# Optimization experiments

Measured on AMD Instinct MI355X. Metric: run time of the kernel, lower is better.

Reference implementation:

```python
import jax, jax.numpy as jnp
import numpy as np

B, C_IN, N_IN, N_OUT = 4, 64, 8192, 8192
D1, F, H = 4, 15, 16384  # d+1, filter_size, max_hash_cnt
C_MID, C_OUT = 64, 64
LEAK = 0.01


def setup_inputs() -> dict:
    key = jax.random.key(0)
    ks = jax.random.split(key, 10)
    features = jax.random.normal(ks[0], (B, C_IN, N_IN), jnp.float32)
    in_barycentric = jax.random.uniform(ks[1], (B, D1, N_IN), dtype=jnp.float32)
    # global flat lattice offsets: local vertex id in [0,H) plus per-batch base b*(H+1)
    local_off = jax.random.randint(ks[2], (B, D1, N_IN), 0, H)
    base = (jnp.arange(B, dtype=jnp.int64) * (H + 1))[:, None, None]
    in_lattice_offset = local_off.astype(jnp.int64) + base
    # neighbor ids in [-1, H); -1 means missing -> maps to zero padding slot after +1
    blur_neighbors = (jax.random.randint(ks[3], (B, F, H), 0, H + 1) - 1).astype(jnp.int64)
    out_barycentric = jax.random.uniform(ks[4], (B, D1, N_OUT), dtype=jnp.float32)
    out_lattice_offset = jax.random.randint(ks[5], (B, D1, N_OUT), 0, H).astype(jnp.int64)
    # blur conv params: layer0 Conv2d(C_IN,C_MID,(F,1)) + LeakyReLU, layer1 Conv2d(C_MID,C_OUT,(1,1)) no relu
    W0 = jax.random.normal(ks[6], (C_MID, C_IN, F), jnp.float32) * 0.05
    b0 = jax.random.normal(ks[7], (C_MID,), jnp.float32) * 0.01
    W1 = jax.random.normal(ks[8], (C_OUT, C_MID), jnp.float32) * 0.1
    b1 = jax.random.normal(ks[9], (C_OUT,), jnp.float32) * 0.01
    bias = jnp.zeros((C_OUT,), jnp.float32)  # slice bias, initialized to zeros as in module
    return dict(features=features, in_barycentric=in_barycentric,
                in_lattice_offset=in_lattice_offset, blur_neighbors=blur_neighbors,
                out_barycentric=out_barycentric, out_lattice_offset=out_lattice_offset,
                W0=W0, b0=b0, W1=W1, b1=b1, bias=bias)


def reference(features, in_barycentric, in_lattice_offset, blur_neighbors,
              out_barycentric, out_lattice_offset, W0, b0, W1, b1, bias):
    b_sz, c_in, n_in = features.shape
    max_hash = blur_neighbors.shape[-1]
    # ---- splat: scatter-sum barycentric-weighted features onto lattice vertices ----
    vals = in_barycentric[:, None, :, :] * features[:, :, None, :]      # (B,C,d1,N)
    vals = vals.transpose(0, 2, 3, 1).reshape(-1, c_in)                  # (B*d1*N, C)
    idx = (in_lattice_offset + 1).reshape(-1)                            # (B*d1*N,)
    splat = jax.ops.segment_sum(vals, idx, num_segments=b_sz * (max_hash + 1))
    splat = splat.reshape(b_sz, max_hash + 1, c_in).transpose(0, 2, 1)   # (B,C,H+1)
    # normalization: splat of all-ones feature
    one_splat = jax.ops.segment_sum(in_barycentric.reshape(-1), idx,
                                    num_segments=b_sz * (max_hash + 1))
    one_splat = one_splat.reshape(b_sz, max_hash + 1)
    splat = splat / (one_splat + 1e-5)[:, None, :]
    # ---- blur: gather F neighbors per vertex, then conv over the filter axis ----
    spread = jax.vmap(lambda s, n: s[:, n])(splat, blur_neighbors + 1)   # (B,C,F,H)
    h0 = jnp.einsum('bcfh,ocf->boh', spread, W0) + b0[None, :, None]     # (B,C_mid,H)
    h0 = jnp.where(h0 > 0, h0, LEAK * h0)                                # LeakyReLU
    feat_blurred = jnp.einsum('boh,po->bph', h0, W1) + b1[None, :, None] # (B,C_out,H)
    # ---- slice: barycentric-weighted gather back to output points ----
    tmp = jax.vmap(lambda f, o: f[:, o])(feat_blurred, out_lattice_offset)  # (B,C_out,d1,N_out)
    sliced = (out_barycentric[:, None, :, :] * tmp).sum(axis=2)
    sliced = sliced + bias[None, :, None]
    return sliced
```

## Files before the change

### kernel.cpp

```cpp
#include <hip/hip_runtime.h>

#define NB 4
#define C_IN 64
#define N_IN 8192
#define N_OUT 8192
#define D1 4
#define FS 15
#define HSZ 16384
#define C_MID 64
#define C_OUT 64
#define LEAK 0.01f
#define CAP 24

#define NVERT (NB*(HSZ+1))

typedef __attribute__((ext_vector_type(8))) short short8;
typedef __attribute__((ext_vector_type(4))) float floatx4;

#define SPLATB_OFF 0
#define SPLATB_FL  (NVERT*32)
#define W0B_OFF    (SPLATB_OFF + SPLATB_FL)
#define W0B_FL     (C_MID*C_IN*FS/2)
#define W1B_OFF    (W0B_OFF + W0B_FL)
#define W1B_FL     (C_OUT*C_MID/2)
#define BREG_OFF   (W1B_OFF + W1B_FL)
#define FEATB_OFF  (BREG_OFF)
#define FEATB_FL   (NB*N_IN*32)
#define CNT_OFF    (FEATB_OFF + FEATB_FL)
#define CNT_FL     (NVERT)
#define ENTID_OFF  (CNT_OFF + CNT_FL)
#define ENT_FL     (NVERT*CAP)
#define ENTW_OFF   (ENTID_OFF + ENT_FL)
#define FB_OFF     (BREG_OFF)
#define FB_FL      (NB*HSZ*32)

__device__ inline ushort f2bf(float x) {
    uint u = __float_as_uint(x);
    return (ushort)((u + 0x7FFF + ((u >> 16) & 1)) >> 16);
}
__device__ inline float bf2f(ushort b) {
    return __uint_as_float(((uint)b) << 16);
}

__global__ __launch_bounds__(256) void transpose_w(const float* __restrict__ W0,
                                                   const float* __restrict__ W1,
                                                   ushort* __restrict__ W0b,
                                                   ushort* __restrict__ W1b) {
    int e = blockIdx.x * 256 + threadIdx.x;
    if (e < C_MID * C_IN * FS) {
        int f = e >> 12;
        int o = (e >> 6) & 63;
        int c = e & 63;
        W0b[e] = f2bf(W0[(o * 64 + c) * FS + f]);
    } else {
        int e2 = e - C_MID * C_IN * FS;
        W1b[e2] = f2bf(W1[e2]);
    }
}

__global__ __launch_bounds__(256) void transpose_feat(const float* __restrict__ feat,
                                                      ushort* __restrict__ featB) {
    __shared__ float t[64 * 65];
    const int b  = blockIdx.x >> 7;
    const int nb = (blockIdx.x & 127) << 6;
    const int l  = threadIdx.x & 63;
    const int g  = threadIdx.x >> 6;
#pragma unroll
    for (int i = 0; i < 16; ++i) {
        int c = g * 16 + i;
        t[c * 65 + l] = feat[((size_t)(b * 64 + c)) * N_IN + nb + l];
    }
    __syncthreads();
#pragma unroll
    for (int i = 0; i < 16; ++i) {
        int n = g * 16 + i;
        featB[((size_t)(b * N_IN) + nb + n) * 64 + l] = f2bf(t[l * 65 + n]);
    }
}

__global__ __launch_bounds__(256) void fill_buckets(const int* __restrict__ off,
                                                    const float* __restrict__ bary,
                                                    int* __restrict__ cnt,
                                                    int* __restrict__ ent_id,
                                                    float* __restrict__ ent_w) {
    int e = blockIdx.x * 256 + threadIdx.x;
    int v = off[e] + 1;
    int n = e % N_IN;
    int b = e / (D1 * N_IN);
    int slot = atomicAdd(&cnt[v], 1);
    if (slot < CAP) {
        ent_id[v * CAP + slot] = b * N_IN + n;
        ent_w [v * CAP + slot] = bary[e];
    }
}

__global__ __launch_bounds__(256) void gather_splat(const ushort* __restrict__ featB,
                                                    const int* __restrict__ cnt,
                                                    const int* __restrict__ ent_id,
                                                    const float* __restrict__ ent_w,
                                                    ushort* __restrict__ splatB) {
    const int v    = blockIdx.x * 4 + (threadIdx.x >> 6);
    const int lane = threadIdx.x & 63;
    int c = cnt[v];
    if (c > CAP) c = CAP;
    float acc = 0.f, sw = 0.f;
    for (int e = 0; e < c; ++e) {
        int   pt = ent_id[v * CAP + e];
        float wt = ent_w [v * CAP + e];
        acc += wt * bf2f(featB[(size_t)pt * 64 + lane]);
        sw  += wt;
    }
    splatB[(size_t)v * 64 + lane] = f2bf(acc / (sw + 1e-5f));
}

#define LSTR 72
__global__ __launch_bounds__(256) void blur_mfma(const ushort* __restrict__ splatB,
                                                 const int* __restrict__ nbr,
                                                 const ushort* __restrict__ W0b,
                                                 const ushort* __restrict__ W1b,
                                                 const float* __restrict__ b0,
                                                 const float* __restrict__ b1,
                                                 ushort* __restrict__ fb) {
    __shared__ ushort As[64 * LSTR];
    __shared__ ushort Xs[64 * LSTR];
    __shared__ ushort Hs[64 * LSTR];

    const int tid = threadIdx.x;
    const int p  = blockIdx.x;
    const int b  = p & 3;
    const int hb = (((p >> 3) << 1) + ((p >> 2) & 1)) << 6;

    const int lane = tid & 63;
    const int w    = tid >> 6;
    const int m    = lane & 15;
    const int q    = lane >> 4;

    const int srow = tid >> 3;
    const int sseg = (tid & 7) * 8;

    floatx4 acc[4] = {};

    for (int f = 0; f < FS; ++f) {
        __syncthreads();
        const ushort* w0f  = W0b + f * 4096;
        const int*    nrow = nbr + ((b * FS) + f) * HSZ + hb;
#pragma unroll
        for (int i = 0; i < 2; ++i) {
            int r = i * 32 + srow;
            *(short8*)&As[r * LSTR + sseg] = *(const short8*)&w0f[r * 64 + sseg];
            int v = nrow[r] + 1;
            *(short8*)&Xs[r * LSTR + sseg] =
                *(const short8*)&splatB[((size_t)(b * (HSZ + 1) + v)) * 64 + sseg];
        }
        __syncthreads();
#pragma unroll
        for (int ch = 0; ch < 2; ++ch) {
            int ko = ch * 32 + q * 8;
            short8 a = *(const short8*)&As[(w * 16 + m) * LSTR + ko];
#pragma unroll
            for (int t = 0; t < 4; ++t) {
                short8 bb = *(const short8*)&Xs[(t * 16 + m) * LSTR + ko];
                acc[t] = __builtin_amdgcn_mfma_f32_16x16x32_bf16(a, bb, acc[t], 0, 0, 0);
            }
        }
    }

    __syncthreads();
#pragma unroll
    for (int i = 0; i < 2; ++i) {
        int r = i * 32 + srow;
        *(short8*)&As[r * LSTR + sseg] = *(const short8*)&W1b[r * 64 + sseg];
    }
    {
        const float4 b0v = *(const float4*)(b0 + w * 16 + q * 4);
#pragma unroll
        for (int t = 0; t < 4; ++t) {
            float v0 = acc[t][0] + b0v.x; v0 = v0 > 0.f ? v0 : LEAK * v0;
            float v1 = acc[t][1] + b0v.y; v1 = v1 > 0.f ? v1 : LEAK * v1;
            float v2 = acc[t][2] + b0v.z; v2 = v2 > 0.f ? v2 : LEAK * v2;
            float v3 = acc[t][3] + b0v.w; v3 = v3 > 0.f ? v3 : LEAK * v3;
            ushort4 hv;
            hv.x = f2bf(v0); hv.y = f2bf(v1); hv.z = f2bf(v2); hv.w = f2bf(v3);
            *(ushort4*)&Hs[(t * 16 + m) * LSTR + w * 16 + q * 4] = hv;
        }
    }
    __syncthreads();

    floatx4 acc2[4] = {};
#pragma unroll
    for (int ch = 0; ch < 2; ++ch) {
        int ko = ch * 32 + q * 8;
        short8 a2 = *(const short8*)&As[(w * 16 + m) * LSTR + ko];
#pragma unroll
        for (int t = 0; t < 4; ++t) {
            short8 b2 = *(const short8*)&Hs[(t * 16 + m) * LSTR + ko];
            acc2[t] = __builtin_amdgcn_mfma_f32_16x16x32_bf16(a2, b2, acc2[t], 0, 0, 0);
        }
    }

    __syncthreads();
    {
        const float4 b1v = *(const float4*)(b1 + w * 16 + q * 4);
#pragma unroll
        for (int t = 0; t < 4; ++t) {
            ushort4 ov;
            ov.x = f2bf(acc2[t][0] + b1v.x);
            ov.y = f2bf(acc2[t][1] + b1v.y);
            ov.z = f2bf(acc2[t][2] + b1v.z);
            ov.w = f2bf(acc2[t][3] + b1v.w);
            *(ushort4*)&Xs[(t * 16 + m) * LSTR + w * 16 + q * 4] = ov;
        }
    }
    __syncthreads();
#pragma unroll
    for (int i = 0; i < 2; ++i) {
        int r = i * 32 + srow;
        *(short8*)&fb[((size_t)(b * HSZ) + hb + r) * 64 + sseg] =
            *(const short8*)&Xs[r * LSTR + sseg];
    }
}

__global__ __launch_bounds__(256) void slice_kernel(const ushort* __restrict__ fb,
                                                    const float* __restrict__ ob,
                                                    const int* __restrict__ off,
                                                    const float* __restrict__ bias,
                                                    float* __restrict__ out) {
    __shared__ float tile[64 * 65];
    const int b    = blockIdx.x >> 7;
    const int nb   = (blockIdx.x & 127) << 6;
    const int lane = threadIdx.x & 63;
    const int w    = threadIdx.x >> 6;

    const float bs = bias[lane];
#pragma unroll 4
    for (int t = 0; t < 16; ++t) {
        int nl = w * 16 + t;
        int n  = nb + nl;
        float acc = bs;
#pragma unroll
        for (int j = 0; j < D1; ++j) {
            float wj = ob[(b * D1 + j) * N_OUT + n];
            int   oj = off[(b * D1 + j) * N_OUT + n];
            acc += wj * bf2f(fb[((size_t)b * HSZ + oj) * 64 + lane]);
        }
        tile[lane * 65 + nl] = acc;
    }
    __syncthreads();
#pragma unroll
    for (int r = 0; r < 16; ++r) {
        int p = w * 16 + r;
        out[((size_t)(b * 64 + p)) * N_OUT + nb + lane] = tile[p * 65 + lane];
    }
}

extern "C" void kernel_launch(void* const* d_in, const int* in_sizes, int n_in,
                              void* d_out, int out_size, void* d_ws, size_t ws_size,
                              hipStream_t stream) {
    const float* features = (const float*)d_in[0];
    const float* in_bary  = (const float*)d_in[1];
    const int*   in_off   = (const int*)d_in[2];
    const int*   nbr      = (const int*)d_in[3];
    const float* out_bary = (const float*)d_in[4];
    const int*   out_off  = (const int*)d_in[5];
    const float* W0       = (const float*)d_in[6];
    const float* b0       = (const float*)d_in[7];
    const float* W1       = (const float*)d_in[8];
    const float* b1       = (const float*)d_in[9];
    const float* bias     = (const float*)d_in[10];

    float*  ws     = (float*)d_ws;
    ushort* splatB = (ushort*)(ws + SPLATB_OFF);
    ushort* W0b    = (ushort*)(ws + W0B_OFF);
    ushort* W1b    = (ushort*)(ws + W1B_OFF);
    ushort* featB  = (ushort*)(ws + FEATB_OFF);
    int*    cnt    = (int*)(ws + CNT_OFF);
    int*    ent_id = (int*)(ws + ENTID_OFF);
    float*  ent_w  = ws + ENTW_OFF;
    ushort* fb     = (ushort*)(ws + FB_OFF);

    hipMemsetAsync(cnt, 0, (size_t)CNT_FL * sizeof(int), stream);

    transpose_w<<<(C_MID * C_IN * FS + C_OUT * C_MID) / 256, 256, 0, stream>>>(W0, W1, W0b, W1b);
    transpose_feat<<<NB * (N_IN / 64), 256, 0, stream>>>(features, featB);
    fill_buckets<<<NB * D1 * N_IN / 256, 256, 0, stream>>>(in_off, in_bary, cnt, ent_id, ent_w);
    gather_splat<<<NVERT / 4, 256, 0, stream>>>(featB, cnt, ent_id, ent_w, splatB);
    blur_mfma<<<NB * (HSZ / 64), 256, 0, stream>>>(splatB, nbr, W0b, W1b, b0, b1, fb);
    slice_kernel<<<NB * (N_OUT / 64), 256, 0, stream>>>(fb, out_bary, out_off, bias, (float*)d_out);
}
```

Before: 149.3 us.

## Merge prep kernels, double-buffer blur MFMA loop, remap block ordering

Three small preprocessing kernels (weight transpose, feature transpose, bucket fill) are folded into one launch, which removes two launch overheads. The blur kernel now double-buffers its weight and gathered-neighbor tiles in shared memory. It prefetches the next filter tap into registers while the MFMAs run, which cuts one barrier per tap, and it adds a launch-bounds occupancy hint. Block-to-(batch, row) mapping changes in both blur and slice, and the LDS row stride changes. The costs are more registers for the prefetch and double the LDS for the tiles.

Measured after the change: 140.5 us. -5.8%, faster.

```diff
diff --git a/kernel.cpp b/kernel.cpp
--- a/kernel.cpp
+++ b/kernel.cpp
@@ -42,55 +42,57 @@
     return __uint_as_float(((uint)b) << 16);
 }
 
-__global__ __launch_bounds__(256) void transpose_w(const float* __restrict__ W0,
-                                                   const float* __restrict__ W1,
-                                                   ushort* __restrict__ W0b,
-                                                   ushort* __restrict__ W1b) {
-    int e = blockIdx.x * 256 + threadIdx.x;
-    if (e < C_MID * C_IN * FS) {
-        int f = e >> 12;
-        int o = (e >> 6) & 63;
-        int c = e & 63;
-        W0b[e] = f2bf(W0[(o * 64 + c) * FS + f]);
+__global__ __launch_bounds__(256) void prep(const float* __restrict__ feat,
+                                            const float* __restrict__ W0,
+                                            const float* __restrict__ W1,
+                                            const int* __restrict__ off,
+                                            const float* __restrict__ bary,
+                                            ushort* __restrict__ featB,
+                                            ushort* __restrict__ W0b,
+                                            ushort* __restrict__ W1b,
+                                            int* __restrict__ cnt,
+                                            int* __restrict__ ent_id,
+                                            float* __restrict__ ent_w) {
+    __shared__ float t[64 * 65];
+    const int blk = blockIdx.x;
+    const int tid = threadIdx.x;
+    if (blk < 512) {
+        const int b  = blk >> 7;
+        const int nb = (blk & 127) << 6;
+        const int l  = tid & 63;
+        const int g  = tid >> 6;
+#pragma unroll
+        for (int i = 0; i < 16; ++i) {
+            int c = g * 16 + i;
+            t[c * 65 + l] = feat[((size_t)(b * 64 + c)) * N_IN + nb + l];
+        }
+        __syncthreads();
+#pragma unroll
+        for (int i = 0; i < 16; ++i) {
+            int n = g * 16 + i;
+            featB[((size_t)(b * N_IN) + nb + n) * 64 + l] = f2bf(t[l * 65 + n]);
+        }
+    } else if (blk < 1024) {
+        int e = (blk - 512) * 256 + tid;
+        int v = off[e] + 1;
+        int n = e % N_IN;
+        int b = e / (D1 * N_IN);
+        int slot = atomicAdd(&cnt[v], 1);
+        if (slot < CAP) {
+            ent_id[v * CAP + slot] = b * N_IN + n;
+            ent_w [v * CAP + slot] = bary[e];
+        }
     } else {
-        int e2 = e - C_MID * C_IN * FS;
-        W1b[e2] = f2bf(W1[e2]);
-    }
-}
-
-__global__ __launch_bounds__(256) void transpose_feat(const float* __restrict__ feat,
-                                                      ushort* __restrict__ featB) {
-    __shared__ float t[64 * 65];
-    const int b  = blockIdx.x >> 7;
-    const int nb = (blockIdx.x & 127) << 6;
-    const int l  = threadIdx.x & 63;
-    const int g  = threadIdx.x >> 6;
-#pragma unroll
-    for (int i = 0; i < 16; ++i) {
-        int c = g * 16 + i;
-        t[c * 65 + l] = feat[((size_t)(b * 64 + c)) * N_IN + nb + l];
-    }
-    __syncthreads();
-#pragma unroll
-    for (int i = 0; i < 16; ++i) {
-        int n = g * 16 + i;
-        featB[((size_t)(b * N_IN) + nb + n) * 64 + l] = f2bf(t[l * 65 + n]);
-    }
-}
-
-__global__ __launch_bounds__(256) void fill_buckets(const int* __restrict__ off,
-                                                    const float* __restrict__ bary,
-                                                    int* __restrict__ cnt,
-                                                    int* __restrict__ ent_id,
-                                                    float* __restrict__ ent_w) {
-    int e = blockIdx.x * 256 + threadIdx.x;
-    int v = off[e] + 1;
-    int n = e % N_IN;
-    int b = e / (D1 * N_IN);
-    int slot = atomicAdd(&cnt[v], 1);
-    if (slot < CAP) {
-        ent_id[v * CAP + slot] = b * N_IN + n;
-        ent_w [v * CAP + slot] = bary[e];
+        int e = (blk - 1024) * 256 + tid;
+        if (e < C_MID * C_IN * FS) {
+            int f = e >> 12;
+            int o = (e >> 6) & 63;
+            int c = e & 63;
+            W0b[e] = f2bf(W0[(o * 64 + c) * FS + f]);
+        } else {
+            int e2 = e - C_MID * C_IN * FS;
+            W1b[e2] = f2bf(W1[e2]);
+        }
     }
 }
 
@@ -113,64 +115,85 @@
     splatB[(size_t)v * 64 + lane] = f2bf(acc / (sw + 1e-5f));
 }
 
-#define LSTR 72
-__global__ __launch_bounds__(256) void blur_mfma(const ushort* __restrict__ splatB,
-                                                 const int* __restrict__ nbr,
-                                                 const ushort* __restrict__ W0b,
-                                                 const ushort* __restrict__ W1b,
-                                                 const float* __restrict__ b0,
-                                                 const float* __restrict__ b1,
-                                                 ushort* __restrict__ fb) {
-    __shared__ ushort As[64 * LSTR];
-    __shared__ ushort Xs[64 * LSTR];
-    __shared__ ushort Hs[64 * LSTR];
+#define LSTR 80
+__global__ __launch_bounds__(256, 4) void blur_mfma(const ushort* __restrict__ splatB,
+                                                    const int* __restrict__ nbr,
+                                                    const ushort* __restrict__ W0b,
+                                                    const ushort* __restrict__ W1b,
+                                                    const float* __restrict__ b0,
+                                                    const float* __restrict__ b1,
+                                                    ushort* __restrict__ fb) {
+    __shared__ ushort As[2][64 * LSTR];
+    __shared__ ushort Xs[2][64 * LSTR];
 
     const int tid = threadIdx.x;
-    const int p  = blockIdx.x;
-    const int b  = p & 3;
-    const int hb = (((p >> 3) << 1) + ((p >> 2) & 1)) << 6;
+    const int p   = blockIdx.x;
+    const int b   = p & 3;
+    const int hb  = (p >> 2) << 6;
 
     const int lane = tid & 63;
     const int w    = tid >> 6;
     const int m    = lane & 15;
     const int q    = lane >> 4;
 
-    const int srow = tid >> 3;
+    const int r0   = tid >> 3;
+    const int r1   = r0 + 32;
     const int sseg = (tid & 7) * 8;
 
+    const int* nbase = nbr + (b * FS) * HSZ + hb;
+    const size_t sbase = (size_t)b * (HSZ + 1) * 64;
+
+    {
+        int v0 = nbase[r0] + 1, v1 = nbase[r1] + 1;
+        *(short8*)&As[0][r0 * LSTR + sseg] = *(const short8*)&W0b[r0 * 64 + sseg];
+        *(short8*)&As[0][r1 * LSTR + sseg] = *(const short8*)&W0b[r1 * 64 + sseg];
+        *(short8*)&Xs[0][r0 * LSTR + sseg] = *(const short8*)&splatB[sbase + (size_t)v0 * 64 + sseg];
+        *(short8*)&Xs[0][r1 * LSTR + sseg] = *(const short8*)&splatB[sbase + (size_t)v1 * 64 + sseg];
+    }
+    int nv0 = nbase[HSZ + r0] + 1;
+    int nv1 = nbase[HSZ + r1] + 1;
+    __syncthreads();
+
     floatx4 acc[4] = {};
 
+#pragma unroll
     for (int f = 0; f < FS; ++f) {
-        __syncthreads();
-        const ushort* w0f  = W0b + f * 4096;
-        const int*    nrow = nbr + ((b * FS) + f) * HSZ + hb;
-#pragma unroll
-        for (int i = 0; i < 2; ++i) {
-            int r = i * 32 + srow;
-            *(short8*)&As[r * LSTR + sseg] = *(const short8*)&w0f[r * 64 + sseg];
-            int v = nrow[r] + 1;
-            *(short8*)&Xs[r * LSTR + sseg] =
-                *(const short8*)&splatB[((size_t)(b * (HSZ + 1) + v)) * 64 + sseg];
-        }
-        __syncthreads();
+        const int cur = f & 1, nxt = cur ^ 1;
+        short8 pa0, pa1, px0, px1;
+        int nn0 = 0, nn1 = 0;
+        if (f < FS - 1) {
+            const ushort* w0n = W0b + (f + 1) * 4096;
+            pa0 = *(const short8*)&w0n[r0 * 64 + sseg];
+            pa1 = *(const short8*)&w0n[r1 * 64 + sseg];
+            px0 = *(const short8*)&splatB[sbase + (size_t)nv0 * 64 + sseg];
+            px1 = *(const short8*)&splatB[sbase + (size_t)nv1 * 64 + sseg];
+            if (f < FS - 2) {
+                nn0 = nbase[(f + 2) * HSZ + r0] + 1;
+                nn1 = nbase[(f + 2) * HSZ + r1] + 1;
+            }
+        }
 #pragma unroll
         for (int ch = 0; ch < 2; ++ch) {
-            int ko = ch * 32 + q * 8;
-            short8 a = *(const short8*)&As[(w * 16 + m) * LSTR + ko];
+            const int ko = ch * 32 + q * 8;
+            short8 a = *(const short8*)&As[cur][(w * 16 + m) * LSTR + ko];
 #pragma unroll
             for (int t = 0; t < 4; ++t) {
-                short8 bb = *(const short8*)&Xs[(t * 16 + m) * LSTR + ko];
+                short8 bb = *(const short8*)&Xs[cur][(t * 16 + m) * LSTR + ko];
                 acc[t] = __builtin_amdgcn_mfma_f32_16x16x32_bf16(a, bb, acc[t], 0, 0, 0);
             }
         }
-    }
-
-    __syncthreads();
-#pragma unroll
-    for (int i = 0; i < 2; ++i) {
-        int r = i * 32 + srow;
-        *(short8*)&As[r * LSTR + sseg] = *(const short8*)&W1b[r * 64 + sseg];
-    }
+        if (f < FS - 1) {
+            *(short8*)&As[nxt][r0 * LSTR + sseg] = pa0;
+            *(short8*)&As[nxt][r1 * LSTR + sseg] = pa1;
+            *(short8*)&Xs[nxt][r0 * LSTR + sseg] = px0;
+            *(short8*)&Xs[nxt][r1 * LSTR + sseg] = px1;
+            nv0 = nn0; nv1 = nn1;
+        }
+        __syncthreads();
+    }
+
+    *(short8*)&As[0][r0 * LSTR + sseg] = *(const short8*)&W1b[r0 * 64 + sseg];
+    *(short8*)&As[0][r1 * LSTR + sseg] = *(const short8*)&W1b[r1 * 64 + sseg];
     {
         const float4 b0v = *(const float4*)(b0 + w * 16 + q * 4);
 #pragma unroll
@@ -181,7 +204,7 @@
             float v3 = acc[t][3] + b0v.w; v3 = v3 > 0.f ? v3 : LEAK * v3;
             ushort4 hv;
             hv.x = f2bf(v0); hv.y = f2bf(v1); hv.z = f2bf(v2); hv.w = f2bf(v3);
-            *(ushort4*)&Hs[(t * 16 + m) * LSTR + w * 16 + q * 4] = hv;
+            *(ushort4*)&Xs[0][(t * 16 + m) * LSTR + w * 16 + q * 4] = hv;
         }
     }
     __syncthreads();
@@ -189,16 +212,15 @@
     floatx4 acc2[4] = {};
 #pragma unroll
     for (int ch = 0; ch < 2; ++ch) {
-        int ko = ch * 32 + q * 8;
-        short8 a2 = *(const short8*)&As[(w * 16 + m) * LSTR + ko];
+        const int ko = ch * 32 + q * 8;
+        short8 a2 = *(const short8*)&As[0][(w * 16 + m) * LSTR + ko];
 #pragma unroll
         for (int t = 0; t < 4; ++t) {
-            short8 b2 = *(const short8*)&Hs[(t * 16 + m) * LSTR + ko];
+            short8 b2 = *(const short8*)&Xs[0][(t * 16 + m) * LSTR + ko];
             acc2[t] = __builtin_amdgcn_mfma_f32_16x16x32_bf16(a2, b2, acc2[t], 0, 0, 0);
         }
     }
 
-    __syncthreads();
     {
         const float4 b1v = *(const float4*)(b1 + w * 16 + q * 4);
 #pragma unroll
@@ -208,16 +230,12 @@
             ov.y = f2bf(acc2[t][1] + b1v.y);
             ov.z = f2bf(acc2[t][2] + b1v.z);
             ov.w = f2bf(acc2[t][3] + b1v.w);
-            *(ushort4*)&Xs[(t * 16 + m) * LSTR + w * 16 + q * 4] = ov;
+            *(ushort4*)&Xs[1][(t * 16 + m) * LSTR + w * 16 + q * 4] = ov;
         }
     }
     __syncthreads();
-#pragma unroll
-    for (int i = 0; i < 2; ++i) {
-        int r = i * 32 + srow;
-        *(short8*)&fb[((size_t)(b * HSZ) + hb + r) * 64 + sseg] =
-            *(const short8*)&Xs[r * LSTR + sseg];
-    }
+    *(short8*)&fb[((size_t)(b * HSZ) + hb + r0) * 64 + sseg] = *(const short8*)&Xs[1][r0 * LSTR + sseg];
+    *(short8*)&fb[((size_t)(b * HSZ) + hb + r1) * 64 + sseg] = *(const short8*)&Xs[1][r1 * LSTR + sseg];
 }
 
 __global__ __launch_bounds__(256) void slice_kernel(const ushort* __restrict__ fb,
@@ -226,8 +244,9 @@
                                                     const float* __restrict__ bias,
                                                     float* __restrict__ out) {
     __shared__ float tile[64 * 65];
-    const int b    = blockIdx.x >> 7;
-    const int nb   = (blockIdx.x & 127) << 6;
+    const int blk  = blockIdx.x;
+    const int b    = blk & 3;
+    const int nb   = (blk >> 2) << 6;
     const int lane = threadIdx.x & 63;
     const int w    = threadIdx.x >> 6;
 
@@ -280,9 +299,8 @@
 
     hipMemsetAsync(cnt, 0, (size_t)CNT_FL * sizeof(int), stream);
 
-    transpose_w<<<(C_MID * C_IN * FS + C_OUT * C_MID) / 256, 256, 0, stream>>>(W0, W1, W0b, W1b);
-    transpose_feat<<<NB * (N_IN / 64), 256, 0, stream>>>(features, featB);
-    fill_buckets<<<NB * D1 * N_IN / 256, 256, 0, stream>>>(in_off, in_bary, cnt, ent_id, ent_w);
+    prep<<<1280, 256, 0, stream>>>(features, W0, W1, in_off, in_bary,
+                                   featB, W0b, W1b, cnt, ent_id, ent_w);
     gather_splat<<<NVERT / 4, 256, 0, stream>>>(featB, cnt, ent_id, ent_w, splatB);
     blur_mfma<<<NB * (HSZ / 64), 256, 0, stream>>>(splatB, nbr, W0b, W1b, b0, b1, fb);
     slice_kernel<<<NB * (N_OUT / 64), 256, 0, stream>>>(fb, out_bary, out_off, bias, (float*)d_out);
```
